# Optimization experiments

Measured on AMD Instinct MI355X. Metric: run time of the kernel, lower is better.

The kernel has to match this reference:

```python
import jax, jax.numpy as jnp
import numpy as np

K = 7        # kernel_size
DIL = 2      # dilation (hardcoded in module)
PAD = 6      # padding, keeps spatial dims with stride=1
G = 8        # groups (group_channels = 16)


def setup_inputs() -> dict:
    key = jax.random.key(0)
    ks = jax.random.split(key, 5)
    B, C, H, W = 4, 128, 64, 64
    Cr = C // 4                      # red_ratio = 4
    KKG = K * K * G                  # 392
    return {
        "x": jax.random.normal(ks[0], (B, C, H, W), jnp.float32),
        "w_reduce": jax.random.normal(ks[1], (Cr, C), jnp.float32) * 0.05,
        "b_reduce": jax.random.normal(ks[2], (Cr,), jnp.float32) * 0.05,
        "w_span": jax.random.normal(ks[3], (KKG, Cr), jnp.float32) * 0.05,
        "b_span": jax.random.normal(ks[4], (KKG,), jnp.float32) * 0.05,
    }


def reference(x, w_reduce, b_reduce, w_span, b_span):
    B, C, H, W = x.shape
    Cg = C // G
    # kernel generation: two 1x1 convs (pointwise matmuls over channel dim)
    red = jnp.einsum('bchw,oc->bohw', x, w_reduce) + b_reduce[None, :, None, None]
    ker = jnp.einsum('bohw,ko->bkhw', red, w_span) + b_span[None, :, None, None]
    ker = ker.reshape(B, G, K * K, H, W)          # [B, G, KK, H, W]
    # unfold: dilated KxK patches, stride 1, 'same' output size
    xp = jnp.pad(x, ((0, 0), (0, 0), (PAD, PAD), (PAD, PAD)))
    patches = jnp.stack(
        [xp[:, :, i * DIL:i * DIL + H, j * DIL:j * DIL + W]
         for i in range(K) for j in range(K)], axis=2)  # [B, C, KK, H, W]
    patches = patches.reshape(B, G, Cg, K * K, H, W)
    # per-pixel dynamic kernel multiply + sum over window
    out = jnp.einsum('bgckhw,bgkhw->bgchw', patches, ker)
    return out.reshape(B, C, H, W)
```

## Files before the change

kernel.cpp:

```cpp
#include <hip/hip_runtime.h>


#define HW 4096
#define NC 128
#define NR 32
#define KK 49
#define PR 76
#define PC 80
#define KSTR 136

typedef __attribute__((ext_vector_type(8))) short short8;
typedef __attribute__((ext_vector_type(4))) float f32x4;

__device__ __forceinline__ unsigned short f2bf(float f) {
  unsigned int u = __float_as_uint(f);
  u = (u + 0x7fffu + ((u >> 16) & 1u)) >> 16;
  return (unsigned short)u;
}
__device__ __forceinline__ float bf2f(unsigned short u) {
  return __uint_as_float(((unsigned int)u) << 16);
}

__global__ __launch_bounds__(256) void red_gen(
    const float* __restrict__ x, const float* __restrict__ w_reduce,
    const float* __restrict__ b_reduce, unsigned short* __restrict__ red_bf,
    float* __restrict__ x_pad) {
  __shared__ float xs[NC][64];
  int t = threadIdx.x;
  int blk = blockIdx.x;
  int b = blk >> 6;
  int row = blk & 63;
  int p0 = row * 64;

  {
    float4 z = make_float4(0.f, 0.f, 0.f, 0.f);
    float* xpb0 = x_pad + (size_t)b * NC * PR * PC;
#pragma unroll
    for (int it = 0; it < 4; ++it) {
      int local = it * 256 + t;
      if (local < 992) {
        int f = row * 992 + local;
        int plane = f / 496;
        int k = f - plane * 496;
        int d;
        if (k < 120) d = k;
        else if (k < 240) d = k - 120 + 70 * 20;
        else {
          int k2 = k - 240;
          int rr = 6 + (k2 >> 2);
          int c4 = k2 & 3;
          d = rr * 20 + ((c4 < 2) ? c4 : 16 + c4);
        }
        *(float4*)(xpb0 + (size_t)plane * PR * PC + d * 4) = z;
      }
    }
  }

  const float* xb = x + b * NC * HW + p0;
  float* xpb = x_pad + ((size_t)(b * NC) * PR + (row + 6)) * PC + 8;
  int fx = t & 15;
  int c0 = t >> 4;
#pragma unroll
  for (int r = 0; r < 8; ++r) {
    int c = c0 + 16 * r;
    float4 v = *(const float4*)(xb + c * HW + fx * 4);
    *(float4*)(&xs[c][fx * 4]) = v;
    *(float4*)(xpb + (size_t)c * PR * PC + fx * 4) = v;
  }
  __syncthreads();

  int px = t & 63;
  int quad = __builtin_amdgcn_readfirstlane(t >> 6);
  const float* wq = w_reduce + quad * 8 * NC;

  float acc[8];
#pragma unroll
  for (int j = 0; j < 8; ++j) acc[j] = b_reduce[quad * 8 + j];

#pragma unroll 8
  for (int k = 0; k < NC; ++k) {
    float xk = xs[k][px];
#pragma unroll
    for (int j = 0; j < 8; ++j) acc[j] += xk * wq[j * NC + k];
  }

  union { short8 v; unsigned short u[8]; } pk;
#pragma unroll
  for (int j = 0; j < 8; ++j) pk.u[j] = f2bf(acc[j]);
  *(short8*)(red_bf + ((size_t)(b * HW) + p0 + px) * NR + quad * 8) = pk.v;
}

__global__ __launch_bounds__(256) void ker_gen(
    const unsigned short* __restrict__ red_bf, const float* __restrict__ w_span,
    const float* __restrict__ b_span, unsigned short* __restrict__ ker) {
  __shared__ short wlds[64 * 32];
  __shared__ float bsl[64];

  int tid = threadIdx.x;
  int blk = blockIdx.x;
  int pxc = blk & 15;
  int g = (blk >> 4) & 7;
  int b = blk >> 7;
  int l = tid & 63;
  int wv = __builtin_amdgcn_readfirstlane(tid >> 6);
  int quad = l >> 4;
  int mn = l & 15;

  const float* wg = w_span + g * KK * NR;
#pragma unroll
  for (int it = 0; it < 8; ++it) {
    int idx = it * 256 + tid;
    wlds[idx] = (idx < KK * NR) ? (short)f2bf(wg[idx]) : (short)0;
  }
  if (tid < 64) bsl[tid] = (tid < KK) ? b_span[g * KK + tid] : 0.f;
  __syncthreads();

  short8 af[4];
#pragma unroll
  for (int tt = 0; tt < 4; ++tt)
    af[tt] = *(const short8*)(&wlds[(tt * 16 + mn) * NR + quad * 8]);

  f32x4 ci[4];
#pragma unroll
  for (int tt = 0; tt < 4; ++tt) {
#pragma unroll
    for (int r = 0; r < 4; ++r) ci[tt][r] = bsl[tt * 16 + quad * 4 + r];
  }

  int px0 = pxc * 256 + wv * 64;
  const unsigned short* rb = red_bf + ((size_t)b * HW + px0 + mn) * NR + quad * 8;
  unsigned short* kp = ker + (size_t)((b * 8 + g) * KK) * HW + px0 + mn;

#pragma unroll
  for (int it = 0; it < 4; ++it) {
    short8 bf = *(const short8*)(rb + (size_t)it * 16 * NR);
    f32x4 d0 = __builtin_amdgcn_mfma_f32_16x16x32_bf16(af[0], bf, ci[0], 0, 0, 0);
    f32x4 d1 = __builtin_amdgcn_mfma_f32_16x16x32_bf16(af[1], bf, ci[1], 0, 0, 0);
    f32x4 d2 = __builtin_amdgcn_mfma_f32_16x16x32_bf16(af[2], bf, ci[2], 0, 0, 0);
    f32x4 d3 = __builtin_amdgcn_mfma_f32_16x16x32_bf16(af[3], bf, ci[3], 0, 0, 0);
    unsigned short* kpi = kp + it * 16;
#pragma unroll
    for (int r = 0; r < 4; ++r) {
      kpi[(size_t)(0 * 16 + quad * 4 + r) * HW] = f2bf(d0[r]);
      kpi[(size_t)(1 * 16 + quad * 4 + r) * HW] = f2bf(d1[r]);
      kpi[(size_t)(2 * 16 + quad * 4 + r) * HW] = f2bf(d2[r]);
    }
    if (quad == 0) kpi[(size_t)48 * HW] = f2bf(d3[0]);
  }
}

__global__ __launch_bounds__(256) void inv_apply(
    const float* __restrict__ x_pad, const unsigned short* __restrict__ ker,
    float* __restrict__ out) {
  __shared__ float kvs[KK * KSTR];
  int blk = blockIdx.x;
  int hp = blk & 31;
  int g = (blk >> 5) & 7;
  int b = blk >> 8;
  int tid = threadIdx.x;
  int h0 = hp * 2;

  const unsigned short* kerbg = ker + ((size_t)(b * 8 + g) * KK) * HW + h0 * 64;
#pragma unroll
  for (int it = 0; it < 4; ++it) {
    int idx = it * 256 + tid;
    if (idx < KK * 16) {
      int tp = idx >> 4;
      int m = idx & 15;
      short8 v = *(const short8*)(kerbg + (size_t)tp * HW + m * 8);
      int pxl = m * 8;
      int r = pxl >> 6, col = pxl & 63;
      float* dst = &kvs[tp * KSTR + r * 68 + col];
      *(float4*)(dst) = make_float4(
          bf2f((unsigned short)v[0]), bf2f((unsigned short)v[1]),
          bf2f((unsigned short)v[2]), bf2f((unsigned short)v[3]));
      *(float4*)(dst + 4) = make_float4(
          bf2f((unsigned short)v[4]), bf2f((unsigned short)v[5]),
          bf2f((unsigned short)v[6]), bf2f((unsigned short)v[7]));
    }
  }
  __syncthreads();

  int c = tid >> 4;
  int sub = tid & 15;
  int r = sub >> 3;
  int oct = sub & 7;
  int h = h0 + r;

  const float* xrow =
      x_pad + ((size_t)(b * NC + g * 16 + c) * PR + h) * PC + 8 * oct;
  float2 a0 = {0.f, 0.f}, a1 = {0.f, 0.f}, a2 = {0.f, 0.f}, a3 = {0.f, 0.f};

#pragma unroll
  for (int i = 0; i < 7; ++i) {
    const float* pr = xrow + 2 * i * PC;
    float xr[24];
#pragma unroll
    for (int m = 0; m < 6; ++m) {
      float4 v = *(const float4*)(pr + 4 * m);
      xr[4 * m] = v.x; xr[4 * m + 1] = v.y;
      xr[4 * m + 2] = v.z; xr[4 * m + 3] = v.w;
    }
#pragma unroll
    for (int j = 0; j < 7; ++j) {
      const float* kb = &kvs[(i * 7 + j) * KSTR + r * 68 + 8 * oct];
      float4 k0 = *(const float4*)(kb);
      float4 k1 = *(const float4*)(kb + 4);
      a0.x = fmaf(xr[2 + 2 * j], k0.x, a0.x);
      a0.y = fmaf(xr[3 + 2 * j], k0.y, a0.y);
      a1.x = fmaf(xr[4 + 2 * j], k0.z, a1.x);
      a1.y = fmaf(xr[5 + 2 * j], k0.w, a1.y);
      a2.x = fmaf(xr[6 + 2 * j], k1.x, a2.x);
      a2.y = fmaf(xr[7 + 2 * j], k1.y, a2.y);
      a3.x = fmaf(xr[8 + 2 * j], k1.z, a3.x);
      a3.y = fmaf(xr[9 + 2 * j], k1.w, a3.y);
    }
  }

  float* op = out + (size_t)(b * NC + g * 16 + c) * HW + h * 64 + 8 * oct;
  *(float4*)op = make_float4(a0.x, a0.y, a1.x, a1.y);
  *(float4*)(op + 4) = make_float4(a2.x, a2.y, a3.x, a3.y);
}

extern "C" void kernel_launch(void* const* d_in, const int* in_sizes, int n_in,
                              void* d_out, int out_size, void* d_ws, size_t ws_size,
                              hipStream_t stream) {
  const float* x        = (const float*)d_in[0];
  const float* w_reduce = (const float*)d_in[1];
  const float* b_reduce = (const float*)d_in[2];
  const float* w_span   = (const float*)d_in[3];
  const float* b_span   = (const float*)d_in[4];
  float* out = (float*)d_out;

  unsigned short* red_bf = (unsigned short*)d_ws;
  float* x_pad = (float*)((char*)d_ws + (1 << 20));
  unsigned short* ker =
      (unsigned short*)(x_pad + (size_t)4 * NC * PR * PC);

  red_gen<<<256, 256, 0, stream>>>(x, w_reduce, b_reduce, red_bf, x_pad);
  ker_gen<<<512, 256, 0, stream>>>(red_bf, w_span, b_span, ker);
  inv_apply<<<1024, 256, 0, stream>>>(x_pad, ker, out);
}
```

Baseline: 100.3 us.

## Fuse dynamic kernel generation into the involution apply kernel

The ker_gen kernel is removed. Each inv_fused block now computes its own 49x128 slice of per-pixel kernel weights with bf16 MFMA straight from red_bf and writes them into LDS. This drops one launch and the global write and re-read of the bf16 kernel tensor. In exchange every block converts w_span to bf16 and stages it in LDS, and LDS use per block grows, which may lower occupancy. The kernel weights now stay in fp32 in LDS instead of being rounded to bf16.

After: 91.29 us. 1.1x faster.

```diff
diff --git a/kernel.cpp b/kernel.cpp
--- a/kernel.cpp
+++ b/kernel.cpp
@@ -16,9 +16,6 @@
   unsigned int u = __float_as_uint(f);
   u = (u + 0x7fffu + ((u >> 16) & 1u)) >> 16;
   return (unsigned short)u;
-}
-__device__ __forceinline__ float bf2f(unsigned short u) {
-  return __uint_as_float(((unsigned int)u) << 16);
 }
 
 __global__ __launch_bounds__(256) void red_gen(
@@ -90,94 +87,67 @@
   *(short8*)(red_bf + ((size_t)(b * HW) + p0 + px) * NR + quad * 8) = pk.v;
 }
 
-__global__ __launch_bounds__(256) void ker_gen(
-    const unsigned short* __restrict__ red_bf, const float* __restrict__ w_span,
-    const float* __restrict__ b_span, unsigned short* __restrict__ ker) {
-  __shared__ short wlds[64 * 32];
-  __shared__ float bsl[64];
-
-  int tid = threadIdx.x;
-  int blk = blockIdx.x;
-  int pxc = blk & 15;
-  int g = (blk >> 4) & 7;
-  int b = blk >> 7;
-  int l = tid & 63;
-  int wv = __builtin_amdgcn_readfirstlane(tid >> 6);
-  int quad = l >> 4;
-  int mn = l & 15;
-
-  const float* wg = w_span + g * KK * NR;
-#pragma unroll
-  for (int it = 0; it < 8; ++it) {
-    int idx = it * 256 + tid;
-    wlds[idx] = (idx < KK * NR) ? (short)f2bf(wg[idx]) : (short)0;
-  }
-  if (tid < 64) bsl[tid] = (tid < KK) ? b_span[g * KK + tid] : 0.f;
-  __syncthreads();
-
-  short8 af[4];
-#pragma unroll
-  for (int tt = 0; tt < 4; ++tt)
-    af[tt] = *(const short8*)(&wlds[(tt * 16 + mn) * NR + quad * 8]);
-
-  f32x4 ci[4];
-#pragma unroll
-  for (int tt = 0; tt < 4; ++tt) {
-#pragma unroll
-    for (int r = 0; r < 4; ++r) ci[tt][r] = bsl[tt * 16 + quad * 4 + r];
-  }
-
-  int px0 = pxc * 256 + wv * 64;
-  const unsigned short* rb = red_bf + ((size_t)b * HW + px0 + mn) * NR + quad * 8;
-  unsigned short* kp = ker + (size_t)((b * 8 + g) * KK) * HW + px0 + mn;
-
-#pragma unroll
-  for (int it = 0; it < 4; ++it) {
-    short8 bf = *(const short8*)(rb + (size_t)it * 16 * NR);
-    f32x4 d0 = __builtin_amdgcn_mfma_f32_16x16x32_bf16(af[0], bf, ci[0], 0, 0, 0);
-    f32x4 d1 = __builtin_amdgcn_mfma_f32_16x16x32_bf16(af[1], bf, ci[1], 0, 0, 0);
-    f32x4 d2 = __builtin_amdgcn_mfma_f32_16x16x32_bf16(af[2], bf, ci[2], 0, 0, 0);
-    f32x4 d3 = __builtin_amdgcn_mfma_f32_16x16x32_bf16(af[3], bf, ci[3], 0, 0, 0);
-    unsigned short* kpi = kp + it * 16;
-#pragma unroll
-    for (int r = 0; r < 4; ++r) {
-      kpi[(size_t)(0 * 16 + quad * 4 + r) * HW] = f2bf(d0[r]);
-      kpi[(size_t)(1 * 16 + quad * 4 + r) * HW] = f2bf(d1[r]);
-      kpi[(size_t)(2 * 16 + quad * 4 + r) * HW] = f2bf(d2[r]);
-    }
-    if (quad == 0) kpi[(size_t)48 * HW] = f2bf(d3[0]);
-  }
-}
-
-__global__ __launch_bounds__(256) void inv_apply(
-    const float* __restrict__ x_pad, const unsigned short* __restrict__ ker,
+__global__ __launch_bounds__(256) void inv_fused(
+    const float* __restrict__ x_pad, const unsigned short* __restrict__ red_bf,
+    const float* __restrict__ w_span, const float* __restrict__ b_span,
     float* __restrict__ out) {
   __shared__ float kvs[KK * KSTR];
+  __shared__ short wlds[64 * NR];
+  __shared__ float bsl[64];
+
   int blk = blockIdx.x;
   int hp = blk & 31;
   int g = (blk >> 5) & 7;
   int b = blk >> 8;
   int tid = threadIdx.x;
   int h0 = hp * 2;
-
-  const unsigned short* kerbg = ker + ((size_t)(b * 8 + g) * KK) * HW + h0 * 64;
-#pragma unroll
-  for (int it = 0; it < 4; ++it) {
+  int p0 = h0 * 64;
+
+  const float* wg = w_span + g * KK * NR;
+#pragma unroll
+  for (int it = 0; it < 8; ++it) {
     int idx = it * 256 + tid;
-    if (idx < KK * 16) {
-      int tp = idx >> 4;
-      int m = idx & 15;
-      short8 v = *(const short8*)(kerbg + (size_t)tp * HW + m * 8);
-      int pxl = m * 8;
-      int r = pxl >> 6, col = pxl & 63;
-      float* dst = &kvs[tp * KSTR + r * 68 + col];
-      *(float4*)(dst) = make_float4(
-          bf2f((unsigned short)v[0]), bf2f((unsigned short)v[1]),
-          bf2f((unsigned short)v[2]), bf2f((unsigned short)v[3]));
-      *(float4*)(dst + 4) = make_float4(
-          bf2f((unsigned short)v[4]), bf2f((unsigned short)v[5]),
-          bf2f((unsigned short)v[6]), bf2f((unsigned short)v[7]));
-    }
+    wlds[idx] = (idx < KK * NR) ? (short)f2bf(wg[idx]) : (short)0;
+  }
+  if (tid < 64) bsl[tid] = (tid < KK) ? b_span[g * KK + tid] : 0.f;
+  __syncthreads();
+
+  int l = tid & 63;
+  int wv = __builtin_amdgcn_readfirstlane(tid >> 6);
+  int quad = l >> 4;
+  int mn = l & 15;
+
+  short8 af[4];
+#pragma unroll
+  for (int tt = 0; tt < 4; ++tt)
+    af[tt] = *(const short8*)(&wlds[(tt * 16 + mn) * NR + quad * 8]);
+
+  f32x4 ci[4];
+#pragma unroll
+  for (int tt = 0; tt < 4; ++tt) {
+#pragma unroll
+    for (int r = 0; r < 4; ++r) ci[tt][r] = bsl[tt * 16 + quad * 4 + r];
+  }
+
+  const unsigned short* rb =
+      red_bf + ((size_t)b * HW + p0 + wv * 32 + mn) * NR + quad * 8;
+#pragma unroll
+  for (int nt = 0; nt < 2; ++nt) {
+    short8 bf = *(const short8*)(rb + (size_t)nt * 16 * NR);
+    f32x4 d0 = __builtin_amdgcn_mfma_f32_16x16x32_bf16(af[0], bf, ci[0], 0, 0, 0);
+    f32x4 d1 = __builtin_amdgcn_mfma_f32_16x16x32_bf16(af[1], bf, ci[1], 0, 0, 0);
+    f32x4 d2 = __builtin_amdgcn_mfma_f32_16x16x32_bf16(af[2], bf, ci[2], 0, 0, 0);
+    f32x4 d3 = __builtin_amdgcn_mfma_f32_16x16x32_bf16(af[3], bf, ci[3], 0, 0, 0);
+    int pxl = wv * 32 + nt * 16 + mn;
+    int r = pxl >> 6, col = pxl & 63;
+    float* dst = &kvs[r * 68 + col];
+#pragma unroll
+    for (int rg = 0; rg < 4; ++rg) {
+      dst[(size_t)(0 * 16 + quad * 4 + rg) * KSTR] = d0[rg];
+      dst[(size_t)(1 * 16 + quad * 4 + rg) * KSTR] = d1[rg];
+      dst[(size_t)(2 * 16 + quad * 4 + rg) * KSTR] = d2[rg];
+    }
+    if (quad == 0) dst[(size_t)48 * KSTR] = d3[0];
   }
   __syncthreads();
 
@@ -234,10 +204,7 @@
 
   unsigned short* red_bf = (unsigned short*)d_ws;
   float* x_pad = (float*)((char*)d_ws + (1 << 20));
-  unsigned short* ker =
-      (unsigned short*)(x_pad + (size_t)4 * NC * PR * PC);
 
   red_gen<<<256, 256, 0, stream>>>(x, w_reduce, b_reduce, red_bf, x_pad);
-  ker_gen<<<512, 256, 0, stream>>>(red_bf, w_span, b_span, ker);
-  inv_apply<<<1024, 256, 0, stream>>>(x_pad, ker, out);
-}
+  inv_fused<<<1024, 256, 0, stream>>>(x_pad, red_bf, w_span, b_span, out);
+}
```
